# Optimization experiments

Hardware: AMD Instinct MI355X
Metric: run time of the kernel (lower is better)

Reference implementation:

```python
import jax, jax.numpy as jnp
import numpy as np

HASH_BINS = 100000
EMB = 64
B = 262144


def _glorot(key, shape):
    fan_in, fan_out = shape[0], shape[-1]
    std = np.sqrt(2.0 / (fan_in + fan_out)).astype(np.float32)
    return jax.random.normal(key, shape, dtype=jnp.float32) * std


def setup_inputs() -> dict:
    key = jax.random.key(0)
    ks = jax.random.split(key, 16)
    return {
        "user_idx": jax.random.randint(ks[0], (B,), 0, HASH_BINS, dtype=jnp.int32),
        "item_idx": jax.random.randint(ks[1], (B,), 0, HASH_BINS, dtype=jnp.int32),
        "user_emb": jax.random.normal(ks[2], (HASH_BINS, EMB), dtype=jnp.float32) * 0.05,
        "item_emb": jax.random.normal(ks[3], (HASH_BINS, EMB), dtype=jnp.float32) * 0.05,
        "lin_w": jax.random.normal(ks[4], (2 * HASH_BINS,), dtype=jnp.float32) * 0.01,
        "lin_b": jnp.zeros((1,), jnp.float32),
        "cross_k": _glorot(ks[5], (2 * EMB, 2 * EMB)),
        "W1": _glorot(ks[6], (2 * EMB, 200)), "b1": jnp.zeros((200,), jnp.float32),
        "W2": _glorot(ks[7], (200, 256)),     "b2": jnp.zeros((256,), jnp.float32),
        "W3": _glorot(ks[8], (256, 200)),     "b3": jnp.zeros((200,), jnp.float32),
        "W4": _glorot(ks[9], (200, 128)),     "b4": jnp.zeros((128,), jnp.float32),
        "W5": _glorot(ks[10], (128, 1)),      "b5": jnp.zeros((1,), jnp.float32),
    }


def reference(user_idx, item_idx, user_emb, item_emb, lin_w, lin_b, cross_k,
              W1, b1, W2, b2, W3, b3, W4, b4, W5, b5):
    # Embedding lookups (flattened + concatenated): [B, 2*EMB]
    emb = jnp.concatenate([user_emb[user_idx], item_emb[item_idx]], axis=1)

    # FM linear term. CategoryEncoding(multi-hot over 2*HASH_BINS) -> Dense(1)
    # is exactly a gather-sum of the dense kernel rows (one user + one item token).
    linear = (lin_w[user_idx] + lin_w[HASH_BINS + item_idx] + lin_b)[:, None]  # [B,1]

    # FM cross term: 0.5 * mean((xK)^2 - x^2 K^2, axis=1)
    xk = emb @ cross_k                      # [B, 128]
    x2k2 = (emb * emb) @ (cross_k * cross_k)
    cross = 0.5 * jnp.mean(xk * xk - x2k2, axis=1, keepdims=True)  # [B,1]

    # Deep MLP (inference: no dropout)
    h = jax.nn.relu(emb @ W1 + b1)
    h = jax.nn.relu(h @ W2 + b2)
    h = jax.nn.relu(h @ W3 + b3)
    h = jax.nn.relu(h @ W4 + b4)
    dnn = h @ W5 + b5                       # [B,1]

    return jax.nn.sigmoid(linear + cross + dnn)
```

## Files before the change

### kernel.cpp

```cpp
#include <hip/hip_runtime.h>

#define HASH_BINS 100000
#define EMBD 64
#define BATCH 262144
#define BM 64
#define SA 264
#define SB 232

typedef __attribute__((ext_vector_type(8))) short short8;
typedef __attribute__((ext_vector_type(4))) float floatx4;
typedef __attribute__((ext_vector_type(4))) unsigned short ushortx4;

static __device__ __forceinline__ unsigned short f2bf(float f) {
  unsigned u = __builtin_bit_cast(unsigned, f);
  u += 0x7fff + ((u >> 16) & 1);
  return (unsigned short)(u >> 16);
}
static __device__ __forceinline__ float bf2f(unsigned short b) {
  return __builtin_bit_cast(float, ((unsigned)b) << 16);
}

__global__ void dfm_prep(const float* __restrict__ K, const float* __restrict__ W1,
                         const float* __restrict__ W2, const float* __restrict__ W3,
                         const float* __restrict__ W4,
                         float* __restrict__ S, unsigned short* __restrict__ Kt,
                         unsigned short* __restrict__ W1t, unsigned short* __restrict__ W2t,
                         unsigned short* __restrict__ W3t, unsigned short* __restrict__ W4t)
{
  int idx = blockIdx.x * 256 + threadIdx.x;
  if (idx < 128) {
    float s = 0.f;
    for (int j = 0; j < 128; j++) { float v = K[idx * 128 + j]; s += v * v; }
    S[idx] = s;
  }
  int i = idx;
  if (i < 16384) {
    int k = i >> 7, n = i & 127;
    Kt[n * 128 + k] = f2bf(K[i]);
  } else if ((i -= 16384) < 25600) {
    int k = i / 200, n = i - k * 200;
    W1t[n * 128 + k] = f2bf(W1[i]);
  } else if ((i -= 25600) < 3072) {
    int n = 200 + (i >> 7), k = i & 127;
    W1t[n * 128 + k] = 0;
  } else if ((i -= 3072) < 51200) {
    int k = i >> 8, n = i & 255;
    W2t[n * 224 + k] = f2bf(W2[i]);
  } else if ((i -= 51200) < 6144) {
    int n = i / 24, k = 200 + (i - n * 24);
    W2t[n * 224 + k] = 0;
  } else if ((i -= 6144) < 51200) {
    int k = i / 200, n = i - k * 200;
    W3t[n * 256 + k] = f2bf(W3[i]);
  } else if ((i -= 51200) < 6144) {
    int n = 200 + (i >> 8), k = i & 255;
    W3t[n * 256 + k] = 0;
  } else if ((i -= 6144) < 25600) {
    int k = i >> 7, n = i & 127;
    W4t[n * 224 + k] = f2bf(W4[i]);
  } else if ((i -= 25600) < 3072) {
    int n = i / 24, k = 200 + (i - n * 24);
    W4t[n * 224 + k] = 0;
  }
}

template <int KP, int CH>
static __device__ __forceinline__ void mfma_pass(const unsigned short* __restrict__ wt,
                                                 int rowOff, const unsigned short* actIn,
                                                 int sin, int m, int qd, floatx4* acc)
{
#pragma unroll
  for (int i = 0; i < CH * 4; i++) acc[i] = {0.f, 0.f, 0.f, 0.f};
#pragma unroll
  for (int ks = 0; ks < KP / 32; ks++) {
    short8 a[4];
#pragma unroll
    for (int rt = 0; rt < 4; rt++)
      a[rt] = *(const short8*)&actIn[(rt * 16 + m) * sin + ks * 32 + qd * 8];
#pragma unroll
    for (int n = 0; n < CH; n++) {
      short8 b = *(const short8*)&wt[(rowOff + n * 16 + m) * KP + ks * 32 + qd * 8];
#pragma unroll
      for (int rt = 0; rt < 4; rt++)
        acc[n * 4 + rt] = __builtin_amdgcn_mfma_f32_16x16x32_bf16(a[rt], b, acc[n * 4 + rt], 0, 0, 0);
    }
  }
}

template <int CH>
static __device__ __forceinline__ void epilogue_relu(const float* __restrict__ bias,
                                                     int colBase, int nreal,
                                                     unsigned short* actOut, int sout,
                                                     int m, int qd, const floatx4* acc)
{
#pragma unroll
  for (int n = 0; n < CH; n++) {
    int col = colBase + n * 16 + m;
    float bv = (col < nreal) ? bias[col] : 0.f;
#pragma unroll
    for (int rt = 0; rt < 4; rt++)
#pragma unroll
      for (int i = 0; i < 4; i++) {
        float v = fmaxf(acc[n * 4 + rt][i] + bv, 0.f);
        actOut[(rt * 16 + qd * 4 + i) * sout + col] = f2bf(v);
      }
  }
}

__global__ __launch_bounds__(256, 2)
void dfm_main(const int* __restrict__ uidx, const int* __restrict__ iidx,
              const float* __restrict__ uemb, const float* __restrict__ iemb,
              const float* __restrict__ linw, const float* __restrict__ linb,
              const float* __restrict__ b1, const float* __restrict__ b2,
              const float* __restrict__ b3, const float* __restrict__ b4,
              const float* __restrict__ W5, const float* __restrict__ b5,
              const float* __restrict__ S, const unsigned short* __restrict__ Wc,
              const unsigned short* __restrict__ W2t, const unsigned short* __restrict__ W3t,
              const unsigned short* __restrict__ W4t,
              float* __restrict__ out)
{
  __shared__ unsigned short actA[BM * SA];
  __shared__ unsigned short actB[BM * SB];
  __shared__ float crosspart[4][BM];
  __shared__ float part[BM][4];
  __shared__ float linrow[BM];

  const int t = threadIdx.x;
  const int lane = t & 63, wave = t >> 6;
  const int m = lane & 15, qd = lane >> 4;
  const int r = t >> 2, c = t & 3;

  {
    int g = blockIdx.x * BM + r;
    int u = uidx[g], it = iidx[g];
    const float* up = uemb + (long)u * EMBD + c * 16;
    const float* ip = iemb + (long)it * EMBD + c * 16;
    float qp = 0.f;
#pragma unroll
    for (int j = 0; j < 16; j += 4) {
      float4 f = *(const float4*)(up + j);
      int col = c * 16 + j;
      float4 sv = *(const float4*)(S + col);
      ushortx4 h = {f2bf(f.x), f2bf(f.y), f2bf(f.z), f2bf(f.w)};
      *(ushortx4*)&actA[r * SA + col] = h;
      qp += f.x * f.x * sv.x + f.y * f.y * sv.y + f.z * f.z * sv.z + f.w * f.w * sv.w;
    }
#pragma unroll
    for (int j = 0; j < 16; j += 4) {
      float4 f = *(const float4*)(ip + j);
      int col = 64 + c * 16 + j;
      float4 sv = *(const float4*)(S + col);
      ushortx4 h = {f2bf(f.x), f2bf(f.y), f2bf(f.z), f2bf(f.w)};
      *(ushortx4*)&actA[r * SA + col] = h;
      qp += f.x * f.x * sv.x + f.y * f.y * sv.y + f.z * f.z * sv.z + f.w * f.w * sv.w;
    }
    part[r][c] = qp;
    if (c == 0) linrow[r] = linw[u] + linw[HASH_BINS + it] + linb[0];
  }
  __syncthreads();

  {
    floatx4 acc[8];
    mfma_pass<128, 2>(Wc, (2 * wave) * 16, actA, SA, m, qd, acc);
    float s[4][4];
#pragma unroll
    for (int rt = 0; rt < 4; rt++)
#pragma unroll
      for (int i = 0; i < 4; i++)
        s[rt][i] = acc[rt][i] * acc[rt][i] + acc[4 + rt][i] * acc[4 + rt][i];
#pragma unroll
    for (int mask = 1; mask < 16; mask <<= 1)
#pragma unroll
      for (int rt = 0; rt < 4; rt++)
#pragma unroll
        for (int i = 0; i < 4; i++)
          s[rt][i] += __shfl_xor(s[rt][i], mask, 64);
    if (m == 0)
#pragma unroll
      for (int rt = 0; rt < 4; rt++)
#pragma unroll
        for (int i = 0; i < 4; i++)
          crosspart[wave][rt * 16 + qd * 4 + i] = s[rt][i];
  }
  {
    int s0 = (wave < 3) ? wave * 4 : 11;
    if (wave < 2) {
      floatx4 acc[16];
      mfma_pass<128, 4>(Wc, 128 + s0 * 16, actA, SA, m, qd, acc);
      epilogue_relu<4>(b1, s0 * 16, 200, actB, SB, m, qd, acc);
    } else {
      floatx4 acc[12];
      mfma_pass<128, 3>(Wc, 128 + s0 * 16, actA, SA, m, qd, acc);
      epilogue_relu<3>(b1, s0 * 16, 200, actB, SB, m, qd, acc);
    }
  }
  __syncthreads();

  {
    floatx4 acc[16];
    mfma_pass<224, 4>(W2t, wave * 4 * 16, actB, SB, m, qd, acc);
    epilogue_relu<4>(b2, wave * 4 * 16, 256, actA, SA, m, qd, acc);
  }
  __syncthreads();

  {
    int s0 = (wave < 3) ? wave * 4 : 11;
    if (wave < 2) {
      floatx4 acc[16];
      mfma_pass<256, 4>(W3t, s0 * 16, actA, SA, m, qd, acc);
      epilogue_relu<4>(b3, s0 * 16, 200, actB, SB, m, qd, acc);
    } else {
      floatx4 acc[12];
      mfma_pass<256, 3>(W3t, s0 * 16, actA, SA, m, qd, acc);
      epilogue_relu<3>(b3, s0 * 16, 200, actB, SB, m, qd, acc);
    }
  }
  __syncthreads();

  {
    floatx4 acc[8];
    mfma_pass<224, 2>(W4t, wave * 2 * 16, actB, SB, m, qd, acc);
    epilogue_relu<2>(b4, wave * 2 * 16, 128, actA, SA, m, qd, acc);
  }
  __syncthreads();

  {
    float qp = part[r][c];
    float d = 0.f;
    const unsigned short* ap = &actA[r * SA + c * 32];
#pragma unroll
    for (int j = 0; j < 4; j++) {
      short8 h = *(const short8*)(ap + j * 8);
      float4 w0 = *(const float4*)(W5 + c * 32 + j * 8);
      float4 w1 = *(const float4*)(W5 + c * 32 + j * 8 + 4);
      d += bf2f((unsigned short)h[0]) * w0.x + bf2f((unsigned short)h[1]) * w0.y +
           bf2f((unsigned short)h[2]) * w0.z + bf2f((unsigned short)h[3]) * w0.w +
           bf2f((unsigned short)h[4]) * w1.x + bf2f((unsigned short)h[5]) * w1.y +
           bf2f((unsigned short)h[6]) * w1.z + bf2f((unsigned short)h[7]) * w1.w;
    }
    const float inv = 0.5f / 128.f;
    part[r][c] = d - inv * qp;
    __syncthreads();
    if (c == 0) {
      float xk2 = crosspart[0][r] + crosspart[1][r] + crosspart[2][r] + crosspart[3][r];
      float logit = linrow[r] + inv * xk2 +
                    part[r][0] + part[r][1] + part[r][2] + part[r][3] + b5[0];
      out[blockIdx.x * BM + r] = 1.f / (1.f + expf(-logit));
    }
  }
}

extern "C" void kernel_launch(void* const* d_in, const int* in_sizes, int n_in,
                              void* d_out, int out_size, void* d_ws, size_t ws_size,
                              hipStream_t stream)
{
  const int*   uidx = (const int*)d_in[0];
  const int*   iidx = (const int*)d_in[1];
  const float* uemb = (const float*)d_in[2];
  const float* iemb = (const float*)d_in[3];
  const float* linw = (const float*)d_in[4];
  const float* linb = (const float*)d_in[5];
  const float* K    = (const float*)d_in[6];
  const float* W1   = (const float*)d_in[7];
  const float* b1   = (const float*)d_in[8];
  const float* W2   = (const float*)d_in[9];
  const float* b2   = (const float*)d_in[10];
  const float* W3   = (const float*)d_in[11];
  const float* b3   = (const float*)d_in[12];
  const float* W4   = (const float*)d_in[13];
  const float* b4   = (const float*)d_in[14];
  const float* W5   = (const float*)d_in[15];
  const float* b5   = (const float*)d_in[16];

  char* w = (char*)d_ws;
  float* S = (float*)w;
  unsigned short* Kt  = (unsigned short*)(w + 512);
  unsigned short* W1t = (unsigned short*)(w + 33280);
  unsigned short* W2t = (unsigned short*)(w + 90624);
  unsigned short* W3t = (unsigned short*)(w + 205312);
  unsigned short* W4t = (unsigned short*)(w + 320000);
  float* out = (float*)d_out;

  dfm_prep<<<736, 256, 0, stream>>>(K, W1, W2, W3, W4, S, Kt, W1t, W2t, W3t, W4t);
  dfm_main<<<BATCH / BM, 256, 0, stream>>>(uidx, iidx, uemb, iemb, linw, linb,
                                           b1, b2, b3, b4, W5, b5,
                                           S, Kt, W2t, W3t, W4t, out);
}
```

Before: 326.6 us.

## Split each 64-row tile across eight waves instead of four

Doubles the block size to 512 threads and redistributes the N-tiles of every MLP layer across 8 waves. Each wave holds fewer accumulators, which lowers register pressure, and the gather and final dot-product stages are split 8 ways per row. Layer 1 is now unevenly balanced (waves 0-3 also compute the cross term), and the larger block with unchanged LDS use may change how many blocks fit on a CU.

```diff
diff --git a/kernel.cpp b/kernel.cpp
--- a/kernel.cpp
+++ b/kernel.cpp
@@ -107,7 +107,7 @@
   }
 }
 
-__global__ __launch_bounds__(256, 2)
+__global__ __launch_bounds__(512)
 void dfm_main(const int* __restrict__ uidx, const int* __restrict__ iidx,
               const float* __restrict__ uemb, const float* __restrict__ iemb,
               const float* __restrict__ linw, const float* __restrict__ linb,
@@ -122,33 +122,33 @@
   __shared__ unsigned short actA[BM * SA];
   __shared__ unsigned short actB[BM * SB];
   __shared__ float crosspart[4][BM];
-  __shared__ float part[BM][4];
+  __shared__ float part[BM][8];
   __shared__ float linrow[BM];
 
   const int t = threadIdx.x;
   const int lane = t & 63, wave = t >> 6;
   const int m = lane & 15, qd = lane >> 4;
-  const int r = t >> 2, c = t & 3;
+  const int r = t >> 3, c = t & 7;
 
   {
     int g = blockIdx.x * BM + r;
     int u = uidx[g], it = iidx[g];
-    const float* up = uemb + (long)u * EMBD + c * 16;
-    const float* ip = iemb + (long)it * EMBD + c * 16;
+    const float* up = uemb + (long)u * EMBD + c * 8;
+    const float* ip = iemb + (long)it * EMBD + c * 8;
     float qp = 0.f;
 #pragma unroll
-    for (int j = 0; j < 16; j += 4) {
+    for (int j = 0; j < 8; j += 4) {
       float4 f = *(const float4*)(up + j);
-      int col = c * 16 + j;
+      int col = c * 8 + j;
       float4 sv = *(const float4*)(S + col);
       ushortx4 h = {f2bf(f.x), f2bf(f.y), f2bf(f.z), f2bf(f.w)};
       *(ushortx4*)&actA[r * SA + col] = h;
       qp += f.x * f.x * sv.x + f.y * f.y * sv.y + f.z * f.z * sv.z + f.w * f.w * sv.w;
     }
 #pragma unroll
-    for (int j = 0; j < 16; j += 4) {
+    for (int j = 0; j < 8; j += 4) {
       float4 f = *(const float4*)(ip + j);
-      int col = 64 + c * 16 + j;
+      int col = 64 + c * 8 + j;
       float4 sv = *(const float4*)(S + col);
       ushortx4 h = {f2bf(f.x), f2bf(f.y), f2bf(f.z), f2bf(f.w)};
       *(ushortx4*)&actA[r * SA + col] = h;
@@ -159,7 +159,7 @@
   }
   __syncthreads();
 
-  {
+  if (wave < 4) {
     floatx4 acc[8];
     mfma_pass<128, 2>(Wc, (2 * wave) * 16, actA, SA, m, qd, acc);
     float s[4][4];
@@ -181,58 +181,57 @@
 #pragma unroll
         for (int i = 0; i < 4; i++)
           crosspart[wave][rt * 16 + qd * 4 + i] = s[rt][i];
-  }
-  {
-    int s0 = (wave < 3) ? wave * 4 : 11;
-    if (wave < 2) {
-      floatx4 acc[16];
-      mfma_pass<128, 4>(Wc, 128 + s0 * 16, actA, SA, m, qd, acc);
-      epilogue_relu<4>(b1, s0 * 16, 200, actB, SB, m, qd, acc);
-    } else {
-      floatx4 acc[12];
-      mfma_pass<128, 3>(Wc, 128 + s0 * 16, actA, SA, m, qd, acc);
-      epilogue_relu<3>(b1, s0 * 16, 200, actB, SB, m, qd, acc);
-    }
-  }
-  __syncthreads();
-
-  {
-    floatx4 acc[16];
-    mfma_pass<224, 4>(W2t, wave * 4 * 16, actB, SB, m, qd, acc);
-    epilogue_relu<4>(b2, wave * 4 * 16, 256, actA, SA, m, qd, acc);
-  }
-  __syncthreads();
-
-  {
-    int s0 = (wave < 3) ? wave * 4 : 11;
-    if (wave < 2) {
-      floatx4 acc[16];
-      mfma_pass<256, 4>(W3t, s0 * 16, actA, SA, m, qd, acc);
-      epilogue_relu<4>(b3, s0 * 16, 200, actB, SB, m, qd, acc);
-    } else {
-      floatx4 acc[12];
-      mfma_pass<256, 3>(W3t, s0 * 16, actA, SA, m, qd, acc);
-      epilogue_relu<3>(b3, s0 * 16, 200, actB, SB, m, qd, acc);
-    }
-  }
-  __syncthreads();
-
-  {
-    floatx4 acc[8];
-    mfma_pass<224, 2>(W4t, wave * 2 * 16, actB, SB, m, qd, acc);
-    epilogue_relu<2>(b4, wave * 2 * 16, 128, actA, SA, m, qd, acc);
+    floatx4 acc2[4];
+    mfma_pass<128, 1>(Wc, 128 + wave * 16, actA, SA, m, qd, acc2);
+    epilogue_relu<1>(b1, wave * 16, 200, actB, SB, m, qd, acc2);
+  } else if (wave < 6) {
+    int s0 = 4 + (wave - 4) * 3;
+    floatx4 acc[12];
+    mfma_pass<128, 3>(Wc, 128 + s0 * 16, actA, SA, m, qd, acc);
+    epilogue_relu<3>(b1, s0 * 16, 200, actB, SB, m, qd, acc);
+  } else {
+    int s0 = 10 + (wave - 6) * 2;
+    floatx4 acc[8];
+    mfma_pass<128, 2>(Wc, 128 + s0 * 16, actA, SA, m, qd, acc);
+    epilogue_relu<2>(b1, s0 * 16, 200, actB, SB, m, qd, acc);
+  }
+  __syncthreads();
+
+  {
+    floatx4 acc[8];
+    mfma_pass<224, 2>(W2t, wave * 2 * 16, actB, SB, m, qd, acc);
+    epilogue_relu<2>(b2, wave * 2 * 16, 256, actA, SA, m, qd, acc);
+  }
+  __syncthreads();
+
+  if (wave < 6) {
+    floatx4 acc[8];
+    mfma_pass<256, 2>(W3t, wave * 2 * 16, actA, SA, m, qd, acc);
+    epilogue_relu<2>(b3, wave * 2 * 16, 200, actB, SB, m, qd, acc);
+  } else {
+    int s0 = 12 + (wave - 6);
+    floatx4 acc[4];
+    mfma_pass<256, 1>(W3t, s0 * 16, actA, SA, m, qd, acc);
+    epilogue_relu<1>(b3, s0 * 16, 200, actB, SB, m, qd, acc);
+  }
+  __syncthreads();
+
+  {
+    floatx4 acc[4];
+    mfma_pass<224, 1>(W4t, wave * 16, actB, SB, m, qd, acc);
+    epilogue_relu<1>(b4, wave * 16, 128, actA, SA, m, qd, acc);
   }
   __syncthreads();
 
   {
     float qp = part[r][c];
     float d = 0.f;
-    const unsigned short* ap = &actA[r * SA + c * 32];
-#pragma unroll
-    for (int j = 0; j < 4; j++) {
+    const unsigned short* ap = &actA[r * SA + c * 16];
+#pragma unroll
+    for (int j = 0; j < 2; j++) {
       short8 h = *(const short8*)(ap + j * 8);
-      float4 w0 = *(const float4*)(W5 + c * 32 + j * 8);
-      float4 w1 = *(const float4*)(W5 + c * 32 + j * 8 + 4);
+      float4 w0 = *(const float4*)(W5 + c * 16 + j * 8);
+      float4 w1 = *(const float4*)(W5 + c * 16 + j * 8 + 4);
       d += bf2f((unsigned short)h[0]) * w0.x + bf2f((unsigned short)h[1]) * w0.y +
            bf2f((unsigned short)h[2]) * w0.z + bf2f((unsigned short)h[3]) * w0.w +
            bf2f((unsigned short)h[4]) * w1.x + bf2f((unsigned short)h[5]) * w1.y +
@@ -243,8 +242,9 @@
     __syncthreads();
     if (c == 0) {
       float xk2 = crosspart[0][r] + crosspart[1][r] + crosspart[2][r] + crosspart[3][r];
-      float logit = linrow[r] + inv * xk2 +
-                    part[r][0] + part[r][1] + part[r][2] + part[r][3] + b5[0];
+      float dnn = part[r][0] + part[r][1] + part[r][2] + part[r][3] +
+                  part[r][4] + part[r][5] + part[r][6] + part[r][7];
+      float logit = linrow[r] + inv * xk2 + dnn + b5[0];
       out[blockIdx.x * BM + r] = 1.f / (1.f + expf(-logit));
     }
   }
@@ -282,7 +282,7 @@
   float* out = (float*)d_out;
 
   dfm_prep<<<736, 256, 0, stream>>>(K, W1, W2, W3, W4, S, Kt, W1t, W2t, W3t, W4t);
-  dfm_main<<<BATCH / BM, 256, 0, stream>>>(uidx, iidx, uemb, iemb, linw, linb,
+  dfm_main<<<BATCH / BM, 512, 0, stream>>>(uidx, iidx, uemb, iemb, linw, linb,
                                            b1, b2, b3, b4, W5, b5,
                                            S, Kt, W2t, W3t, W4t, out);
 }
```

Result: faster. 289.3 us (-11.4%).
